# Kernel tuning notes

Measured on AMD Instinct MI355X. Metric: run time of the kernel, lower is better.

Reference implementation:

```python
import jax, jax.numpy as jnp
import numpy as np

B, L, C = 8, 3136, 192
HEADS, HEAD_CH = 3, 64
EPS = 1e-5


def _dwconv(x, w, s):
    # depthwise 3x3 conv, SAME padding; w: [3,3,1,C], feature_group_count=C
    return jax.lax.conv_general_dilated(
        x, w, (s, s), 'SAME',
        dimension_numbers=('NHWC', 'HWIO', 'NHWC'),
        feature_group_count=x.shape[-1])


def _proj(x, dw, scale, bias, mean, var, pw, s):
    # depthwise conv -> BN (inference, running stats) -> 1x1 pointwise conv
    h = _dwconv(x, dw, s)
    h = (h - mean) * jax.lax.rsqrt(var + EPS) * scale + bias
    return jax.lax.conv_general_dilated(
        h, pw, (1, 1), 'SAME',
        dimension_numbers=('NHWC', 'HWIO', 'NHWC'))


def setup_inputs() -> dict:
    key = jax.random.key(0)
    ks = jax.random.split(key, 7)
    d = {'x': jax.random.normal(ks[0], (B, L, C), jnp.float32)}
    for i, p in enumerate(['q', 'k', 'v']):
        d[p + '_dw'] = jax.random.normal(ks[i + 1], (3, 3, 1, C), jnp.float32) * 0.1
        d[p + '_scale'] = jnp.ones((C,), jnp.float32)
        d[p + '_bias'] = jnp.zeros((C,), jnp.float32)
        d[p + '_mean'] = jnp.zeros((C,), jnp.float32)
        d[p + '_var'] = jnp.ones((C,), jnp.float32)
        d[p + '_pw'] = jax.random.normal(ks[i + 4], (1, 1, C, HEADS * HEAD_CH), jnp.float32) * 0.05
    d['is_training'] = 0  # inference: BN uses running averages
    return d


def reference(x, q_dw, q_scale, q_bias, q_mean, q_var, q_pw,
              k_dw, k_scale, k_bias, k_mean, k_var, k_pw,
              v_dw, v_scale, v_bias, v_mean, v_var, v_pw,
              is_training):
    S = int(np.ceil(np.sqrt(L)))  # 56; L is a perfect square, so no token padding
    xi = x.reshape(B, S, S, C)
    q = _proj(xi, q_dw, q_scale, q_bias, q_mean, q_var, q_pw, 1)  # [B,56,56,192]
    k = _proj(xi, k_dw, k_scale, k_bias, k_mean, k_var, k_pw, 2)  # [B,28,28,192]
    v = _proj(xi, v_dw, v_scale, v_bias, v_mean, v_var, v_pw, 2)  # [B,28,28,192]
    q = q.reshape(B, -1, HEADS, HEAD_CH) / jnp.sqrt(jnp.float32(HEAD_CH))
    k = k.reshape(B, -1, HEADS, HEAD_CH)
    v = v.reshape(B, -1, HEADS, HEAD_CH)
    attn = jax.nn.softmax(jnp.einsum('bqhd,bkhd->bhqk', q, k), axis=-1)
    o = jnp.einsum('bhqk,bkhd->bqhd', attn, v)
    # num_heads*head_ch == out_ch -> plain head merge, no output projection
    return o.reshape(B, L, HEADS * HEAD_CH)
```

## Files before the change

### kernel.cpp

```cpp
#include <hip/hip_runtime.h>
#include <cmath>

#define EPS_BN 1e-5f

typedef __bf16 bf16;
typedef __bf16 bf16x4 __attribute__((ext_vector_type(4)));
typedef __bf16 bf16x8 __attribute__((ext_vector_type(8)));
typedef float  f32x4  __attribute__((ext_vector_type(4)));

__device__ __forceinline__ void dma16(const bf16* g, bf16* l) {
    __builtin_amdgcn_global_load_lds(
        (const __attribute__((address_space(1))) void*)g,
        (__attribute__((address_space(3))) void*)l, 16, 0, 0);
}

__global__ __launch_bounds__(256) void conv_all_kernel(
    const float* __restrict__ x,
    const float* __restrict__ qdw, const float* __restrict__ qscale,
    const float* __restrict__ qbias, const float* __restrict__ qmean,
    const float* __restrict__ qvar,
    const float* __restrict__ kdw, const float* __restrict__ kscale,
    const float* __restrict__ kbias, const float* __restrict__ kmean,
    const float* __restrict__ kvar,
    const float* __restrict__ vdw, const float* __restrict__ vscale,
    const float* __restrict__ vbias, const float* __restrict__ vmean,
    const float* __restrict__ vvar,
    const float* __restrict__ qpw, const float* __restrict__ kpw,
    const float* __restrict__ vpw,
    bf16* __restrict__ qhi, bf16* __restrict__ qlo,
    bf16* __restrict__ khi, bf16* __restrict__ klo,
    bf16* __restrict__ vhi, bf16* __restrict__ vlo,
    bf16* __restrict__ wt) {
    const int WW = 56, C = 192;
    int bid = blockIdx.x;

    if (bid < 4704) {
        int idx = bid * 256 + threadIdx.x;
        int p  = idx / 48;
        int c4 = (idx - p * 48) * 4;
        int b  = p / 3136;
        int rem = p - b * 3136;
        int oy = rem / 56;
        int ox = rem - oy * 56;
        const float* xb = x + (size_t)b * 3136 * C;

        float4 sc = *(const float4*)&qscale[c4];
        float4 vr = *(const float4*)&qvar[c4];
        float4 bi = *(const float4*)&qbias[c4];
        float4 mn = *(const float4*)&qmean[c4];
        float aA[4] = {sc.x * rsqrtf(vr.x + EPS_BN), sc.y * rsqrtf(vr.y + EPS_BN),
                       sc.z * rsqrtf(vr.z + EPS_BN), sc.w * rsqrtf(vr.w + EPS_BN)};
        float aB[4] = {bi.x - mn.x * aA[0], bi.y - mn.y * aA[1],
                       bi.z - mn.z * aA[2], bi.w - mn.w * aA[3]};
        float s[4] = {0.f, 0.f, 0.f, 0.f};
#pragma unroll
        for (int ky = 0; ky < 3; ky++) {
            int iy = oy + ky - 1;
            bool yok = (iy >= 0) && (iy < 56);
#pragma unroll
            for (int kx = 0; kx < 3; kx++) {
                int ix = ox + kx - 1;
                if (yok && ix >= 0 && ix < WW) {
                    float4 xv = *(const float4*)&xb[((size_t)iy * WW + ix) * C + c4];
                    float4 wv = *(const float4*)&qdw[(ky * 3 + kx) * C + c4];
                    s[0] += xv.x * wv.x; s[1] += xv.y * wv.y;
                    s[2] += xv.z * wv.z; s[3] += xv.w * wv.w;
                }
            }
        }
        bf16x4 hv, lv;
#pragma unroll
        for (int j = 0; j < 4; j++) {
            float av = s[j] * aA[j] + aB[j];
            bf16 hh = (bf16)av;
            hv[j] = hh;
            lv[j] = (bf16)(av - (float)hh);
        }
        *(bf16x4*)&qhi[(size_t)p * C + c4] = hv;
        *(bf16x4*)&qlo[(size_t)p * C + c4] = lv;
    } else if (bid < 5880) {
        int idx = (bid - 4704) * 256 + threadIdx.x;
        int p  = idx / 48;
        int c4 = (idx - p * 48) * 4;
        int b  = p / 784;
        int rem = p - b * 784;
        int oy = rem / 28;
        int ox = rem - oy * 28;
        const float* xb = x + (size_t)b * 3136 * C;

        float ks[4] = {0.f, 0.f, 0.f, 0.f};
        float vs[4] = {0.f, 0.f, 0.f, 0.f};
#pragma unroll
        for (int ky = 0; ky < 3; ky++) {
            int iy = oy * 2 + ky;
            bool yok = iy < 56;
#pragma unroll
            for (int kx = 0; kx < 3; kx++) {
                int ix = ox * 2 + kx;
                if (yok && ix < WW) {
                    float4 xv = *(const float4*)&xb[((size_t)iy * WW + ix) * C + c4];
                    float4 kw = *(const float4*)&kdw[(ky * 3 + kx) * C + c4];
                    float4 vw = *(const float4*)&vdw[(ky * 3 + kx) * C + c4];
                    ks[0] += xv.x * kw.x; ks[1] += xv.y * kw.y;
                    ks[2] += xv.z * kw.z; ks[3] += xv.w * kw.w;
                    vs[0] += xv.x * vw.x; vs[1] += xv.y * vw.y;
                    vs[2] += xv.z * vw.z; vs[3] += xv.w * vw.w;
                }
            }
        }
        float4 ksc = *(const float4*)&kscale[c4];
        float4 kvr = *(const float4*)&kvar[c4];
        float4 kbi = *(const float4*)&kbias[c4];
        float4 kmn = *(const float4*)&kmean[c4];
        float4 vsc = *(const float4*)&vscale[c4];
        float4 vvr = *(const float4*)&vvar[c4];
        float4 vbi = *(const float4*)&vbias[c4];
        float4 vmn = *(const float4*)&vmean[c4];
        float kA[4] = {ksc.x * rsqrtf(kvr.x + EPS_BN), ksc.y * rsqrtf(kvr.y + EPS_BN),
                       ksc.z * rsqrtf(kvr.z + EPS_BN), ksc.w * rsqrtf(kvr.w + EPS_BN)};
        float kB[4] = {kbi.x - kmn.x * kA[0], kbi.y - kmn.y * kA[1],
                       kbi.z - kmn.z * kA[2], kbi.w - kmn.w * kA[3]};
        float vA[4] = {vsc.x * rsqrtf(vvr.x + EPS_BN), vsc.y * rsqrtf(vvr.y + EPS_BN),
                       vsc.z * rsqrtf(vvr.z + EPS_BN), vsc.w * rsqrtf(vvr.w + EPS_BN)};
        float vB[4] = {vbi.x - vmn.x * vA[0], vbi.y - vmn.y * vA[1],
                       vbi.z - vmn.z * vA[2], vbi.w - vmn.w * vA[3]};
        bf16x4 kh, kl, vh, vl;
#pragma unroll
        for (int j = 0; j < 4; j++) {
            float kf = ks[j] * kA[j] + kB[j];
            float vf = vs[j] * vA[j] + vB[j];
            bf16 h1 = (bf16)kf; kh[j] = h1; kl[j] = (bf16)(kf - (float)h1);
            bf16 h2 = (bf16)vf; vh[j] = h2; vl[j] = (bf16)(vf - (float)h2);
        }
        *(bf16x4*)&khi[(size_t)p * C + c4] = kh;
        *(bf16x4*)&klo[(size_t)p * C + c4] = kl;
        *(bf16x4*)&vhi[(size_t)p * C + c4] = vh;
        *(bf16x4*)&vlo[(size_t)p * C + c4] = vl;
    } else {
        int idx = (bid - 5880) * 256 + threadIdx.x;
        if (idx < 3 * 36864) {
            int mat = idx / 36864, r = idx % 36864;
            int n = r / 192, k = r - n * 192;
            const float* src = (mat == 0) ? qpw : (mat == 1) ? kpw : vpw;
            wt[idx] = (bf16)src[k * 192 + n];
        }
    }
}

__global__ __launch_bounds__(256) void gemm_all_kernel(
    const bf16* __restrict__ qhi, const bf16* __restrict__ qlo,
    const bf16* __restrict__ khi, const bf16* __restrict__ klo,
    const bf16* __restrict__ vhi, const bf16* __restrict__ vlo,
    const bf16* __restrict__ wt,
    bf16* __restrict__ qbuf, bf16* __restrict__ kbuf, bf16* __restrict__ vtbuf) {
    __shared__ bf16 Ws[96][200];
    int t = threadIdx.x;
    int bid = blockIdx.x;

    int mode, mt, nh;
    const bf16 *Ahi, *Alo, *Wsrc;
    if (bid < 784)      { mode = 0; mt = bid >> 1;         nh = bid & 1;
                          Ahi = qhi; Alo = qlo; Wsrc = wt; }
    else if (bid < 980) { mode = 1; int r = bid - 784; mt = r >> 1; nh = r & 1;
                          Ahi = khi; Alo = klo; Wsrc = wt + 36864; }
    else                { mode = 2; int r = bid - 980; mt = r >> 1; nh = r & 1;
                          Ahi = vhi; Alo = vlo; Wsrc = wt + 73728; }
    int n0 = nh * 96;

#pragma unroll
    for (int it = 0; it < 9; it++) {
        int idx = it * 256 + t;
        int n = idx / 24, ck = idx - n * 24;
        *(uint4*)&Ws[n][ck * 8] = *(const uint4*)&Wsrc[(size_t)(n0 + n) * 192 + ck * 8];
    }
    __syncthreads();

    int lane = t & 63, wid = t >> 6;
    int l16 = lane & 15, quad = lane >> 4;
    int wrow = wid * 16;
    int m0 = mt * 64;

    f32x4 acc[6];
#pragma unroll
    for (int n = 0; n < 6; n++) acc[n] = f32x4{0.f, 0.f, 0.f, 0.f};

    const bf16* arh = Ahi + (size_t)(m0 + wrow + l16) * 192;
    const bf16* arl = Alo + (size_t)(m0 + wrow + l16) * 192;
#pragma unroll
    for (int kc = 0; kc < 6; kc++) {
        bf16x8 ah = *(const bf16x8*)(arh + kc * 32 + quad * 8);
        bf16x8 al = *(const bf16x8*)(arl + kc * 32 + quad * 8);
#pragma unroll
        for (int n = 0; n < 6; n++) {
            bf16x8 bfr = *(const bf16x8*)&Ws[n * 16 + l16][kc * 32 + quad * 8];
            acc[n] = __builtin_amdgcn_mfma_f32_16x16x32_bf16(al, bfr, acc[n], 0, 0, 0);
            acc[n] = __builtin_amdgcn_mfma_f32_16x16x32_bf16(ah, bfr, acc[n], 0, 0, 0);
        }
    }

    if (mode == 2) {
#pragma unroll
        for (int reg = 0; reg < 4; reg++) {
            int row = m0 + wrow + quad * 4 + reg;
            int b = row / 784;
            int loc = row - b * 784;
#pragma unroll
            for (int n = 0; n < 6; n++) {
                int col = n0 + n * 16 + l16;
                int h = col >> 6, d = col & 63;
                vtbuf[(((size_t)b * 3 + h) * 64 + d) * 784 + loc] = (bf16)acc[n][reg];
            }
        }
    } else {
        bf16* outp = (mode == 0) ? qbuf : kbuf;
        const float s = (mode == 0) ? 0.125f : 1.0f;
#pragma unroll
        for (int reg = 0; reg < 4; reg++) {
            size_t row = m0 + wrow + quad * 4 + reg;
#pragma unroll
            for (int n = 0; n < 6; n++)
                outp[row * 192 + n0 + n * 16 + l16] = (bf16)(acc[n][reg] * s);
        }
    }
}

__global__ __launch_bounds__(256)
__attribute__((amdgpu_waves_per_eu(3, 3)))
void attn3_kernel(const bf16* __restrict__ qb,
                  const bf16* __restrict__ kb,
                  const bf16* __restrict__ vtb,
                  float* __restrict__ out) {
    const int LQ = 3136, LK = 784, C = 192;
    int qt = blockIdx.x, h = blockIdx.y, b = blockIdx.z;

    __shared__ bf16 Ks[2][7168];
    __shared__ bf16 Ps[64][136];

    int t    = threadIdx.x;
    int lane = t & 63;
    int wid  = t >> 6;
    int l16  = lane & 15;
    int quad = lane >> 4;
    int wrow = wid * 16;

    if (lane < 32) {
        int row = wrow + (lane >> 1);
        int part = lane & 1;
        *(uint4*)&Ps[row][112 + part * 8] = make_uint4(0u, 0u, 0u, 0u);
    }

    const bf16* kbase  = kb + (size_t)b * LK * C + h * 64;
    const bf16* vtbase = vtb + ((size_t)(b * 3 + h)) * 64 * LK;

    const bf16* ksrc = kbase + (lane >> 3) * C + (((lane & 7) ^ (lane >> 3)) * 8);

    for (int s = wid; s < 14; s += 4)
        dma16(ksrc + s * 8 * C, &Ks[0][s * 512]);

    bf16x8 qfrag[2];
    {
        const bf16* qrow = qb + ((size_t)b * LQ + qt * 64 + wrow + l16) * C + h * 64;
        qfrag[0] = *(const bf16x8*)(qrow + quad * 8);
        qfrag[1] = *(const bf16x8*)(qrow + 32 + quad * 8);
    }

    const bf16* vcbase = vtbase + (size_t)l16 * LK + quad * 8;
    bf16x8 vfrag[4][4];
#pragma unroll
    for (int kk = 0; kk < 4; kk++)
#pragma unroll
        for (int dt = 0; dt < 4; dt++)
            vfrag[kk][dt] = *(const bf16x8*)(vcbase + (size_t)(dt * 16) * LK + kk * 32);
#pragma unroll
    for (int kk = 0; kk < 4; kk++)
#pragma unroll
        for (int dt = 0; dt < 4; dt++)
            asm volatile("" :: "v"(vfrag[kk][dt]));

    int kA0 = l16 * 64 + (((quad    ) ^ (l16 & 7)) * 8);
    int kA1 = l16 * 64 + (((quad + 4) ^ (l16 & 7)) * 8);

    float m_run = -INFINITY, l_run = 0.f;
    f32x4 o_acc[4];
#pragma unroll
    for (int dt = 0; dt < 4; dt++) o_acc[dt] = f32x4{0.f, 0.f, 0.f, 0.f};

    __syncthreads();

    for (int c = 0; c < 7; c++) {
        const int cur = c & 1, nxt = cur ^ 1;

        if (c < 6) {
            const bf16* kn = ksrc + (size_t)(c + 1) * 112 * C;
            for (int s = wid; s < 14; s += 4)
                dma16(kn + s * 8 * C, &Ks[nxt][s * 512]);
        }

        f32x4 st[7];
#pragma unroll
        for (int kb7 = 0; kb7 < 7; kb7++) st[kb7] = f32x4{0.f, 0.f, 0.f, 0.f};
#pragma unroll
        for (int kk = 0; kk < 2; kk++) {
            int kA = (kk == 0) ? kA0 : kA1;
#pragma unroll
            for (int kb7 = 0; kb7 < 7; kb7++) {
                bf16x8 afrag = *(const bf16x8*)&Ks[cur][kb7 * 1024 + kA];
                st[kb7] = __builtin_amdgcn_mfma_f32_16x16x32_bf16(afrag, qfrag[kk], st[kb7], 0, 0, 0);
            }
        }

        float mx = -INFINITY;
#pragma unroll
        for (int kb7 = 0; kb7 < 7; kb7++)
#pragma unroll
            for (int r = 0; r < 4; r++) mx = fmaxf(mx, st[kb7][r]);
        mx = fmaxf(mx, __shfl_xor(mx, 16, 64));
        mx = fmaxf(mx, __shfl_xor(mx, 32, 64));
        float m_new = fmaxf(m_run, mx);
        float alpha = __expf(m_run - m_new);

        float rs = 0.f;
#pragma unroll
        for (int kb7 = 0; kb7 < 7; kb7++) {
            bf16x4 pv;
#pragma unroll
            for (int r = 0; r < 4; r++) {
                float p = __expf(st[kb7][r] - m_new);
                rs += p;
                pv[r] = (bf16)p;
            }
            *(bf16x4*)&Ps[wrow + l16][kb7 * 16 + quad * 4] = pv;
        }
        rs += __shfl_xor(rs, 16, 64);
        rs += __shfl_xor(rs, 32, 64);
        l_run = l_run * alpha + rs;
        m_run = m_new;
#pragma unroll
        for (int dt = 0; dt < 4; dt++)
#pragma unroll
            for (int r = 0; r < 4; r++) o_acc[dt][r] *= alpha;

#pragma unroll
        for (int kk = 0; kk < 4; kk++) {
            bf16x8 pfrag = *(const bf16x8*)&Ps[wrow + l16][kk * 32 + quad * 8];
#pragma unroll
            for (int dt = 0; dt < 4; dt++)
                o_acc[dt] = __builtin_amdgcn_mfma_f32_16x16x32_bf16(vfrag[kk][dt], pfrag, o_acc[dt], 0, 0, 0);
        }

        if (c < 6) {
            const bf16* vn = vcbase + (size_t)(c + 1) * 112;
#pragma unroll
            for (int kk = 0; kk < 4; kk++)
#pragma unroll
                for (int dt = 0; dt < 4; dt++)
                    vfrag[kk][dt] = *(const bf16x8*)(vn + (size_t)(dt * 16) * LK + kk * 32);
#pragma unroll
            for (int kk = 0; kk < 4; kk++)
#pragma unroll
                for (int dt = 0; dt < 4; dt++)
                    asm volatile("" :: "v"(vfrag[kk][dt]));
        }

        __syncthreads();
    }

    float invl = 1.f / l_run;
    float* ob = out + ((size_t)b * LQ + qt * 64 + wrow + l16) * C + h * 64;
#pragma unroll
    for (int dt = 0; dt < 4; dt++) {
        float4 v4 = {o_acc[dt][0] * invl, o_acc[dt][1] * invl,
                     o_acc[dt][2] * invl, o_acc[dt][3] * invl};
        *(float4*)(ob + dt * 16 + quad * 4) = v4;
    }
}

extern "C" void kernel_launch(void* const* d_in, const int* in_sizes, int n_in,
                              void* d_out, int out_size, void* d_ws, size_t ws_size,
                              hipStream_t stream) {
    const float* x = (const float*)d_in[0];

    const float* q_dw = (const float*)d_in[1];
    const float* q_scale = (const float*)d_in[2];
    const float* q_bias = (const float*)d_in[3];
    const float* q_mean = (const float*)d_in[4];
    const float* q_var = (const float*)d_in[5];
    const float* q_pw = (const float*)d_in[6];

    const float* k_dw = (const float*)d_in[7];
    const float* k_scale = (const float*)d_in[8];
    const float* k_bias = (const float*)d_in[9];
    const float* k_mean = (const float*)d_in[10];
    const float* k_var = (const float*)d_in[11];
    const float* k_pw = (const float*)d_in[12];

    const float* v_dw = (const float*)d_in[13];
    const float* v_scale = (const float*)d_in[14];
    const float* v_bias = (const float*)d_in[15];
    const float* v_mean = (const float*)d_in[16];
    const float* v_var = (const float*)d_in[17];
    const float* v_pw = (const float*)d_in[18];

    float* out = (float*)d_out;

    char* ws = (char*)d_ws;
    bf16* qhi = (bf16*)(ws);
    bf16* qlo = (bf16*)(ws + 9633792);
    bf16* khi = (bf16*)(ws + 19267584);
    bf16* klo = (bf16*)(ws + 21676032);
    bf16* vhi = (bf16*)(ws + 24084480);
    bf16* vlo = (bf16*)(ws + 26492928);
    bf16* qbuf = (bf16*)(ws + 28901376);
    bf16* kbuf = (bf16*)(ws + 38535168);
    bf16* vtbuf = (bf16*)(ws + 40943616);
    bf16* wt = (bf16*)(ws + 43352064);

    conv_all_kernel<<<6312, 256, 0, stream>>>(
        x,
        q_dw, q_scale, q_bias, q_mean, q_var,
        k_dw, k_scale, k_bias, k_mean, k_var,
        v_dw, v_scale, v_bias, v_mean, v_var,
        q_pw, k_pw, v_pw,
        qhi, qlo, khi, klo, vhi, vlo, wt);

    gemm_all_kernel<<<1176, 256, 0, stream>>>(
        qhi, qlo, khi, klo, vhi, vlo, wt, qbuf, kbuf, vtbuf);

    attn3_kernel<<<dim3(49, 3, 8), 256, 0, stream>>>(qbuf, kbuf, vtbuf, out);
}
```

Before: 196.8 us.

## Stage V tiles in LDS via async DMA instead of register prefetch

```diff
diff --git a/kernel.cpp b/kernel.cpp
--- a/kernel.cpp
+++ b/kernel.cpp
@@ -225,7 +225,7 @@
 }
 
 __global__ __launch_bounds__(256)
-__attribute__((amdgpu_waves_per_eu(3, 3)))
+__attribute__((amdgpu_waves_per_eu(2, 2)))
 void attn3_kernel(const bf16* __restrict__ qb,
                   const bf16* __restrict__ kb,
                   const bf16* __restrict__ vtb,
@@ -234,6 +234,7 @@
     int qt = blockIdx.x, h = blockIdx.y, b = blockIdx.z;
 
     __shared__ bf16 Ks[2][7168];
+    __shared__ bf16 Vts[8192];
     __shared__ bf16 Ps[64][136];
 
     int t    = threadIdx.x;
@@ -254,6 +255,16 @@
 
     const bf16* ksrc = kbase + (lane >> 3) * C + (((lane & 7) ^ (lane >> 3)) * 8);
 
+    int voff[4];
+#pragma unroll
+    for (int i = 0; i < 4; i++) {
+        int s = wid + 4 * i;
+        int j = s * 64 + lane;
+        int row = j >> 4;
+        int l = (j & 15) ^ (row & 7);
+        voff[i] = row * LK + l * 8;
+    }
+
     for (int s = wid; s < 14; s += 4)
         dma16(ksrc + s * 8 * C, &Ks[0][s * 512]);
 
@@ -264,19 +275,6 @@
         qfrag[1] = *(const bf16x8*)(qrow + 32 + quad * 8);
     }
 
-    const bf16* vcbase = vtbase + (size_t)l16 * LK + quad * 8;
-    bf16x8 vfrag[4][4];
-#pragma unroll
-    for (int kk = 0; kk < 4; kk++)
-#pragma unroll
-        for (int dt = 0; dt < 4; dt++)
-            vfrag[kk][dt] = *(const bf16x8*)(vcbase + (size_t)(dt * 16) * LK + kk * 32);
-#pragma unroll
-    for (int kk = 0; kk < 4; kk++)
-#pragma unroll
-        for (int dt = 0; dt < 4; dt++)
-            asm volatile("" :: "v"(vfrag[kk][dt]));
-
     int kA0 = l16 * 64 + (((quad    ) ^ (l16 & 7)) * 8);
     int kA1 = l16 * 64 + (((quad + 4) ^ (l16 & 7)) * 8);
 
@@ -289,12 +287,19 @@
 
     for (int c = 0; c < 7; c++) {
         const int cur = c & 1, nxt = cur ^ 1;
+        const int j0 = c * 112;
+
+#pragma unroll
+        for (int i = 0; i < 4; i++)
+            dma16(vtbase + j0 + voff[i], Vts + (wid + 4 * i) * 512);
+        __builtin_amdgcn_sched_barrier(0);
 
         if (c < 6) {
             const bf16* kn = ksrc + (size_t)(c + 1) * 112 * C;
             for (int s = wid; s < 14; s += 4)
                 dma16(kn + s * 8 * C, &Ks[nxt][s * 512]);
         }
+        __builtin_amdgcn_sched_barrier(0);
 
         f32x4 st[7];
 #pragma unroll
@@ -340,26 +345,25 @@
 #pragma unroll
             for (int r = 0; r < 4; r++) o_acc[dt][r] *= alpha;
 
+        if (c < 6) {
+            if (wid < 2) asm volatile("s_waitcnt vmcnt(4)" ::: "memory");
+            else         asm volatile("s_waitcnt vmcnt(3)" ::: "memory");
+        } else {
+            asm volatile("s_waitcnt vmcnt(0)" ::: "memory");
+        }
+        __builtin_amdgcn_s_barrier();
+        __builtin_amdgcn_sched_barrier(0);
+
+        int vx = l16 & 7;
 #pragma unroll
         for (int kk = 0; kk < 4; kk++) {
             bf16x8 pfrag = *(const bf16x8*)&Ps[wrow + l16][kk * 32 + quad * 8];
 #pragma unroll
-            for (int dt = 0; dt < 4; dt++)
-                o_acc[dt] = __builtin_amdgcn_mfma_f32_16x16x32_bf16(vfrag[kk][dt], pfrag, o_acc[dt], 0, 0, 0);
-        }
-
-        if (c < 6) {
-            const bf16* vn = vcbase + (size_t)(c + 1) * 112;
-#pragma unroll
-            for (int kk = 0; kk < 4; kk++)
-#pragma unroll
-                for (int dt = 0; dt < 4; dt++)
-                    vfrag[kk][dt] = *(const bf16x8*)(vn + (size_t)(dt * 16) * LK + kk * 32);
-#pragma unroll
-            for (int kk = 0; kk < 4; kk++)
-#pragma unroll
-                for (int dt = 0; dt < 4; dt++)
-                    asm volatile("" :: "v"(vfrag[kk][dt]));
+            for (int dt = 0; dt < 4; dt++) {
+                bf16x8 vfrag = *(const bf16x8*)&Vts[(dt * 16 + l16) * 128
+                                                   + (((kk * 4 + quad) ^ vx) * 8)];
+                o_acc[dt] = __builtin_amdgcn_mfma_f32_16x16x32_bf16(vfrag, pfrag, o_acc[dt], 0, 0, 0);
+            }
         }
 
         __syncthreads();
```

After: 184.2 us. -6.4%, faster.
